# Kernel optimization log

Hardware: AMD Instinct MI355X
Metric: run time of the kernel (lower is better)

## Reference

```python
import jax, jax.numpy as jnp
import numpy as np

N_NODES = 100000
N_EDGES = 1600000
HIDDEN = 128
STEPS = 4
N_GRAPHS = 64


def setup_inputs() -> dict:
    key = jax.random.key(0)
    ks = jax.random.split(key, 8)
    x = jax.random.normal(ks[0], (N_NODES, HIDDEN), dtype=jnp.float32)
    edge_index = jax.random.randint(ks[1], (2, N_EDGES), 0, N_NODES, dtype=jnp.int64)
    batch = jnp.sort(jax.random.randint(ks[2], (N_NODES,), 0, N_GRAPHS, dtype=jnp.int64))
    s = 1.0 / np.sqrt(HIDDEN)
    weight = jax.random.normal(ks[3], (STEPS, HIDDEN, HIDDEN), dtype=jnp.float32) * s
    w_ih = jax.random.normal(ks[4], (3 * HIDDEN, HIDDEN), dtype=jnp.float32) * s
    w_hh = jax.random.normal(ks[5], (3 * HIDDEN, HIDDEN), dtype=jnp.float32) * s
    b_ih = jnp.zeros((3 * HIDDEN,), dtype=jnp.float32)
    b_hh = jnp.zeros((3 * HIDDEN,), dtype=jnp.float32)
    return {"x": x, "edge_index": edge_index, "batch": batch,
            "weight": weight, "w_ih": w_ih, "w_hh": w_hh,
            "b_ih": b_ih, "b_hh": b_hh}


def _gru_cell(m, h, w_ih, w_hh, b_ih, b_hh):
    # PyTorch GRUCell: gates ordered (r, z, n)
    gi = m @ w_ih.T + b_ih  # [N, 3H]
    gh = h @ w_hh.T + b_hh  # [N, 3H]
    i_r, i_z, i_n = jnp.split(gi, 3, axis=-1)
    h_r, h_z, h_n = jnp.split(gh, 3, axis=-1)
    r = jax.nn.sigmoid(i_r + h_r)
    z = jax.nn.sigmoid(i_z + h_z)
    n = jnp.tanh(i_n + r * h_n)
    return (1.0 - z) * n + z * h


def reference(x, edge_index, batch, weight, w_ih, w_hh, b_ih, b_hh):
    src, dst = edge_index[0], edge_index[1]
    h = x
    for i in range(STEPS):
        m = h @ weight[i]  # [N, H]
        # message = m[src] scattered (add) into dst
        aggr = jax.ops.segment_sum(m[src], dst, num_segments=N_NODES)
        h = _gru_cell(aggr, h, w_ih, w_hh, b_ih, b_hh)
    h = jax.nn.relu(h)
    # global mean pool per graph
    sums = jax.ops.segment_sum(h, batch, num_segments=N_GRAPHS)  # [G, H]
    counts = jax.ops.segment_sum(jnp.ones((N_NODES,), h.dtype), batch, num_segments=N_GRAPHS)
    return sums / jnp.maximum(counts, 1.0)[:, None]
```

## Files before the change

### kernel.cpp

```cpp
#include <hip/hip_runtime.h>

#define N_NODES  100000
#define N_EDGES  1600000
#define HIDDEN   128
#define STEPS    4
#define N_GRAPHS 64
#define NBUCK    256
#define BWID     391
#define BCAP     7168

typedef unsigned short u16;
typedef unsigned int   u32;
typedef unsigned long long u64;
typedef __attribute__((ext_vector_type(8))) short bf16x8;
typedef __attribute__((ext_vector_type(4))) float f32x4;
typedef __attribute__((ext_vector_type(2))) float f32x2;

__device__ inline u16 f2bf(float f) {
  u32 u = __float_as_uint(f);
  u = (u + 0x7FFFu + ((u >> 16) & 1u)) >> 16;
  return (u16)u;
}
__device__ inline float bf2f(u16 b) { return __uint_as_float(((u32)b) << 16); }

__device__ inline float rcp_f(float x) { return __builtin_amdgcn_rcpf(x); }
__device__ inline float sig_f(float x) { return rcp_f(1.f + __expf(-x)); }
__device__ inline float tanh_f(float x) { return 1.f - 2.f * rcp_f(1.f + __expf(2.f * x)); }

__device__ inline u32 swz(u32 b) { return b ^ (((b >> 8) & 7u) << 4); }

__global__ __launch_bounds__(1024) void k_part(const int* __restrict__ esrc,
                                               const int* __restrict__ edst,
                                               int* __restrict__ gcursor,
                                               u32* __restrict__ ebuf) {
  __shared__ int hist[16][NBUCK];
  __shared__ int base[16][NBUCK];
  int tid = threadIdx.x;
  int wv  = tid >> 6;
  #pragma unroll
  for (int i = 0; i < 4; ++i) ((int*)hist)[tid + i * 1024] = 0;
  __syncthreads();
  int e0 = blockIdx.x * 4096;
  int sv[4], dv[4], bk[4], rk[4];
  #pragma unroll
  for (int i = 0; i < 4; ++i) {
    int e = e0 + i * 1024 + tid;
    if (e < N_EDGES) {
      sv[i] = esrc[e];
      dv[i] = edst[e];
      bk[i] = (int)((u32)dv[i] / (u32)BWID);
      rk[i] = atomicAdd(&hist[wv][bk[i]], 1);
    } else bk[i] = -1;
  }
  __syncthreads();
  if (tid < NBUCK) {
    int c[16];
    int sum = 0;
    #pragma unroll
    for (int w = 0; w < 16; ++w) { c[w] = hist[w][tid]; sum += c[w]; }
    int g = atomicAdd(&gcursor[tid], sum);
    #pragma unroll
    for (int w = 0; w < 16; ++w) { base[w][tid] = g; g += c[w]; }
  }
  __syncthreads();
  #pragma unroll
  for (int i = 0; i < 4; ++i) {
    if (bk[i] >= 0) {
      int pos = bk[i] * BCAP + base[wv][bk[i]] + rk[i];
      ebuf[pos] = ((u32)(dv[i] - bk[i] * BWID) << 17) | (u32)sv[i];
    }
  }
}

__global__ void k_bscan(const int* __restrict__ gcursor, int* __restrict__ ebase,
                        float* __restrict__ acc) {
  __shared__ int buf[NBUCK];
  int t = threadIdx.x;
  int v = gcursor[t];
  buf[t] = v;
  __syncthreads();
  for (int off = 1; off < NBUCK; off <<= 1) {
    int u = 0;
    if (t >= off) u = buf[t - off];
    __syncthreads();
    buf[t] += u;
    __syncthreads();
  }
  ebase[t] = buf[t] - v;
  if (t == NBUCK - 1) ebase[NBUCK] = buf[t];
  for (int i = t; i < N_GRAPHS * HIDDEN; i += NBUCK) acc[i] = 0.f;
}

__global__ __launch_bounds__(1024) void k_csr(const u32* __restrict__ ebuf,
                                              const int* __restrict__ ebase,
                                              int* __restrict__ offs,
                                              int* __restrict__ csr) {
  __shared__ int lcnt[512];
  __shared__ int lofs[512];
  int b = blockIdx.x, tid = threadIdx.x;
  int n0 = b * BWID;
  int n1 = min(n0 + BWID, N_NODES);
  int nn = n1 - n0;
  int e0 = ebase[b];
  int cnt = ebase[b + 1] - e0;
  const u32* ebase_p = ebuf + (size_t)b * BCAP;
  if (tid < 512) lcnt[tid] = 0;
  __syncthreads();
  for (int e = tid; e < cnt; e += 1024) {
    int dst = (int)(ebase_p[e] >> 17);
    atomicAdd(&lcnt[dst], 1);
  }
  __syncthreads();
  if (tid < 512) lofs[tid] = lcnt[tid];
  __syncthreads();
  for (int off = 1; off < 512; off <<= 1) {
    int v = 0;
    if (tid < 512 && tid >= off) v = lofs[tid - off];
    __syncthreads();
    if (tid < 512 && tid >= off) lofs[tid] += v;
    __syncthreads();
  }
  int nodeoff = 0;
  if (tid < 512) nodeoff = e0 + lofs[tid] - lcnt[tid];
  if (tid < 512) lofs[tid] = nodeoff;
  if (tid < nn) offs[n0 + tid] = nodeoff;
  if (b == 0 && tid == 0) offs[N_NODES] = N_EDGES;
  __syncthreads();
  for (int e = tid; e < cnt; e += 1024) {
    u32 p = ebase_p[e];
    int src = (int)(p & 0x1FFFFu);
    int dst = (int)(p >> 17);
    int pos = atomicAdd(&lofs[dst], 1);
    csr[pos] = src;
  }
}

__global__ void k_wb(const float* __restrict__ W, const float* __restrict__ w_ih,
                     const float* __restrict__ w_hh, u16* __restrict__ bsw) {
  __shared__ float wrow[128];
  int b = blockIdx.x, st = b >> 8, k = b & 255, t = threadIdx.x;
  if (k < 128) wrow[t] = W[(st * 128 + k) * 128 + t];
  __syncthreads();
  int kc = k >> 5, quad = (k >> 3) & 3, kl = k & 7;
  u16* base = bsw + (size_t)st * 131072 + kc * 16384;
  #pragma unroll
  for (int gq = 0; gq < 4; ++gq) {
    int c = gq * 128 + t;
    float v;
    if (k < 128) {
      if (c < 384) {
        const float* wr = w_ih + c * 128;
        float sacc = 0.f;
        for (int j = 0; j < 128; ++j) sacc += wrow[j] * wr[j];
        v = sacc;
      } else v = 0.f;
    } else {
      int kk = k - 128;
      if (c < 256)      v = w_hh[c * 128 + kk];
      else if (c < 384) v = 0.f;
      else              v = w_hh[(c - 128) * 128 + kk];
    }
    int gi = c >> 7, cw = c & 127;
    int wv = cw >> 5, hu = (cw >> 4) & 1, nl = c & 15;
    int slot = wv * 8 + gi * 2 + hu;
    base[(slot * 4 + quad) * 128 + nl * 8 + kl] = f2bf(v);
  }
}

__global__ void k_convert(const float* __restrict__ x, u16* __restrict__ h0,
                          u16* __restrict__ h1) {
  int i = (blockIdx.x * 256 + threadIdx.x) * 4;
  float4 v = *(const float4*)(x + i);
  u16 o[4] = {f2bf(v.x), f2bf(v.y), f2bf(v.z), f2bf(v.w)};
  *(uint2*)(h0 + i) = *(uint2*)o;
  if (blockIdx.x == 0) {
    int t = threadIdx.x;
    if (t < 64)       ((u32*)(h0 + (size_t)N_NODES * 128))[t] = 0;
    else if (t < 128) ((u32*)(h1 + (size_t)N_NODES * 128))[t - 64] = 0;
  }
}

__device__ inline void acc8(f32x2* a, uint4 p) {
  f32x2 v;
  v.x = __uint_as_float(p.x << 16); v.y = __uint_as_float(p.x & 0xffff0000u);
  a[0] += v;
  v.x = __uint_as_float(p.y << 16); v.y = __uint_as_float(p.y & 0xffff0000u);
  a[1] += v;
  v.x = __uint_as_float(p.z << 16); v.y = __uint_as_float(p.z & 0xffff0000u);
  a[2] += v;
  v.x = __uint_as_float(p.w << 16); v.y = __uint_as_float(p.w & 0xffff0000u);
  a[3] += v;
}
__device__ inline uint4 ldrow(const char* hb, u32 off) {
  return *(const uint4*)(hb + off);
}

__global__ __launch_bounds__(256, 3) void k_fused(
    const u16* __restrict__ h_mat, const int* __restrict__ csr,
    const int* __restrict__ offs, const u16* __restrict__ bsw,
    const float* __restrict__ b_ih, const float* __restrict__ b_hh,
    u16* __restrict__ h_out) {
  __shared__ u16 Asw[8192];
  char* lds = (char*)Asw;

  const int tid  = threadIdx.x;
  const int wave = tid >> 6;
  const int lane = tid & 63;
  const int nl   = lane & 15;
  const int quad = lane >> 4;
  const int row0 = blockIdx.x * 32;

  {
    int snl = tid & 15, squad = (tid >> 4) & 3, w = tid >> 6;
    int g = w & 1;
    const u16* row = h_mat + (size_t)(row0 + g * 16 + snl) * 128;
    #pragma unroll
    for (int kk = 0; kk < 2; ++kk) {
      int kc2 = (w >> 1) * 2 + kk;
      uint4 v = *(const uint4*)(row + kc2 * 32 + squad * 8);
      u32 b = (u32)(((g * 8 + 4 + kc2) * 4 + squad) * 256 + snl * 16);
      *(uint4*)(lds + swz(b)) = v;
    }
  }

  {
    const char* hb = (const char*)h_mat;
    const int q   = quad;
    const u32 co  = (u32)(nl * 16);
    #pragma unroll 1
    for (int p = 0; p < 4; ++p) {
      int nA = wave * 8 + p * 2;
      int node = row0 + nA;
      int o0 = offs[node], o1 = offs[node + 1], o2 = offs[node + 2];
      f32x2 aA[4], aB[4];
      #pragma unroll
      for (int r = 0; r < 4; ++r) { aA[r] = (f32x2){0.f, 0.f}; aB[r] = (f32x2){0.f, 0.f}; }
      int jA = o0 + q, jB = o1 + q;
      int dmax = max(o1 - o0, o2 - o1);
      int iters = (dmax + 15) >> 4;
      #pragma unroll 1
      for (int t = 0; t < iters; ++t) {
        u32 sa[4], sb[4];
        #pragma unroll
        for (int k = 0; k < 4; ++k) {
          int jj = jA + 4 * k;
          u32 sv = (u32)csr[jj < o1 ? jj : 0];
          sa[k] = (jj < o1) ? sv : (u32)N_NODES;
          jj = jB + 4 * k;
          sv = (u32)csr[jj < o2 ? jj : 0];
          sb[k] = (jj < o2) ? sv : (u32)N_NODES;
        }
        uint4 pa0 = ldrow(hb, (sa[0] << 8) | co);
        uint4 pa1 = ldrow(hb, (sa[1] << 8) | co);
        uint4 pa2 = ldrow(hb, (sa[2] << 8) | co);
        uint4 pa3 = ldrow(hb, (sa[3] << 8) | co);
        uint4 pb0 = ldrow(hb, (sb[0] << 8) | co);
        uint4 pb1 = ldrow(hb, (sb[1] << 8) | co);
        uint4 pb2 = ldrow(hb, (sb[2] << 8) | co);
        uint4 pb3 = ldrow(hb, (sb[3] << 8) | co);
        acc8(aA, pa0); acc8(aA, pa1); acc8(aA, pa2); acc8(aA, pa3);
        acc8(aB, pb0); acc8(aB, pb1); acc8(aB, pb2); acc8(aB, pb3);
        jA += 16; jB += 16;
      }
      #pragma unroll
      for (int r = 0; r < 4; ++r) {
        aA[r].x += __shfl_xor(aA[r].x, 16); aA[r].x += __shfl_xor(aA[r].x, 32);
        aA[r].y += __shfl_xor(aA[r].y, 16); aA[r].y += __shfl_xor(aA[r].y, 32);
        aB[r].x += __shfl_xor(aB[r].x, 16); aB[r].x += __shfl_xor(aB[r].x, 32);
        aB[r].y += __shfl_xor(aB[r].y, 16); aB[r].y += __shfl_xor(aB[r].y, 32);
      }
      if (q < 2) {
        f32x2 w0 = q ? aB[0] : aA[0];
        f32x2 w1 = q ? aB[1] : aA[1];
        f32x2 w2 = q ? aB[2] : aA[2];
        f32x2 w3 = q ? aB[3] : aA[3];
        uint4 o;
        o.x = (u32)f2bf(w0.x) | ((u32)f2bf(w0.y) << 16);
        o.y = (u32)f2bf(w1.x) | ((u32)f2bf(w1.y) << 16);
        o.z = (u32)f2bf(w2.x) | ((u32)f2bf(w2.y) << 16);
        o.w = (u32)f2bf(w3.x) | ((u32)f2bf(w3.y) << 16);
        int n = nA + q, g = n >> 4, snl = n & 15;
        u32 b = (u32)(g * 8192 + nl * 256 + snl * 16);
        *(uint4*)(lds + swz(b)) = o;
      }
    }
  }
  __syncthreads();

  const u16* bp = bsw + wave * 8 * 512 + lane * 8;

  f32x4 acc[2][8];
  #pragma unroll
  for (int g = 0; g < 2; ++g)
    #pragma unroll
    for (int u = 0; u < 8; ++u) acc[g][u] = (f32x4){0.f, 0.f, 0.f, 0.f};

  bf16x8 b0[6], b1[6], b2[6];
  #pragma unroll
  for (int i = 0; i < 6; ++i) b0[i] = *(const bf16x8*)(bp + i * 512);
  #pragma unroll
  for (int i = 0; i < 6; ++i) b1[i] = *(const bf16x8*)(bp + 16384 + i * 512);

  #pragma unroll
  for (int kc = 0; kc < 8; ++kc) {
    if (kc < 6) {
      #pragma unroll
      for (int i = 0; i < 6; ++i) {
        int us = (kc + 2 < 4) ? i : (i < 4 ? i : i + 2);
        b2[i] = *(const bf16x8*)(bp + (kc + 2) * 16384 + us * 512);
      }
    }
    bf16x8 a0 = *(const bf16x8*)(lds + swz((u32)(kc * 1024 + lane * 16)));
    bf16x8 a1 = *(const bf16x8*)(lds + swz((u32)((8 + kc) * 1024 + lane * 16)));
    #pragma unroll
    for (int i = 0; i < 6; ++i) {
      int u = (kc < 4) ? i : (i < 4 ? i : i + 2);
      acc[0][u] = __builtin_amdgcn_mfma_f32_16x16x32_bf16(a0, b0[i], acc[0][u], 0, 0, 0);
      acc[1][u] = __builtin_amdgcn_mfma_f32_16x16x32_bf16(a1, b0[i], acc[1][u], 0, 0, 0);
    }
    #pragma unroll
    for (int i = 0; i < 6; ++i) { b0[i] = b1[i]; b1[i] = b2[i]; }
  }

  float bias[8];
  #pragma unroll
  for (int u = 0; u < 8; ++u) {
    int gi = u >> 1, hu = u & 1;
    int cw = wave * 32 + hu * 16 + nl;
    bias[u] = (gi == 0) ? b_ih[cw] + b_hh[cw]
            : (gi == 1) ? b_ih[128 + cw] + b_hh[128 + cw]
            : (gi == 2) ? b_ih[256 + cw]
                        : b_hh[256 + cw];
  }

  #pragma unroll
  for (int g = 0; g < 2; ++g) {
    #pragma unroll
    for (int hu = 0; hu < 2; ++hu) {
      int cw = wave * 32 + hu * 16 + nl;
      u32 hslot = (u32)((g * 8 + 4 + wave) * 4 + ((hu * 2 + (nl >> 3)) & 3));
      #pragma unroll
      for (int i = 0; i < 4; ++i) {
        int m = quad * 4 + i;
        float rv = sig_f(acc[g][0 + hu][i] + bias[0 + hu]);
        float zv = sig_f(acc[g][2 + hu][i] + bias[2 + hu]);
        float iv = acc[g][4 + hu][i] + bias[4 + hu];
        float hn = acc[g][6 + hu][i] + bias[6 + hu];
        u32 hb2 = hslot * 256 + (u32)m * 16 + (u32)(nl & 7) * 2;
        float hv = bf2f(*(const u16*)(lds + swz(hb2)));
        float n  = tanh_f(iv + rv * hn);
        float o  = n + zv * (hv - n);
        h_out[(size_t)(row0 + g * 16 + m) * 128 + cw] = f2bf(o);
      }
    }
  }
}

__global__ void k_pool_partial(const u16* __restrict__ h, const int* __restrict__ batch,
                               float* __restrict__ acc) {
  int t = threadIdx.x;
  int node0 = blockIdx.x * 125;
  int node1 = node0 + 125;
  int cur = batch[node0];
  float sum = 0.f;
  for (int r = node0; r < node1; ++r) {
    int g = batch[r];
    if (g != cur) {
      atomicAdd(&acc[cur * 128 + t], sum);
      sum = 0.f;
      cur = g;
    }
    sum += fmaxf(bf2f(h[(size_t)r * 128 + t]), 0.f);
  }
  atomicAdd(&acc[cur * 128 + t], sum);
}

__global__ void k_pool_div(const float* __restrict__ acc, const int* __restrict__ batch,
                           float* __restrict__ out) {
  __shared__ int se[2];
  int g = blockIdx.x, t = threadIdx.x;
  if (t < 2) {
    int target = g + t;
    int lo = 0, hi = N_NODES;
    while (lo < hi) { int mid = (lo + hi) >> 1; if (batch[mid] < target) lo = mid + 1; else hi = mid; }
    se[t] = lo;
  }
  __syncthreads();
  int cnt = se[1] - se[0];
  out[g * 128 + t] = acc[g * 128 + t] / (float)(cnt > 0 ? cnt : 1);
}

extern "C" void kernel_launch(void* const* d_in, const int* in_sizes, int n_in,
                              void* d_out, int out_size, void* d_ws, size_t ws_size,
                              hipStream_t stream) {
  const float* x     = (const float*)d_in[0];
  const int*   edges = (const int*)d_in[1];
  const int*   batch = (const int*)d_in[2];
  const float* W     = (const float*)d_in[3];
  const float* w_ih  = (const float*)d_in[4];
  const float* w_hh  = (const float*)d_in[5];
  const float* b_ih  = (const float*)d_in[6];
  const float* b_hh  = (const float*)d_in[7];
  float* out = (float*)d_out;

  char* w = (char*)d_ws;
  u16* buf0    = (u16*)(w);
  u16* buf1    = (u16*)(w + 25600256);
  u16* bsw     = (u16*)(w + 51200512);
  float* acc   = (float*)(w + 52249088);
  int* offs    = (int*)(w + 52281856);
  int* gcursor = (int*)(w + 52682240);
  int* ebase   = (int*)(w + 52683264);
  int* csr     = (int*)(w + 52684800);
  u32* ebuf    = (u32*)buf1;

  const int* esrc = edges;
  const int* edst = edges + N_EDGES;

  hipMemsetAsync(gcursor, 0, NBUCK * sizeof(int), stream);
  k_part<<<391, 1024, 0, stream>>>(esrc, edst, gcursor, ebuf);
  k_bscan<<<1, NBUCK, 0, stream>>>(gcursor, ebase, acc);
  k_csr<<<NBUCK, 1024, 0, stream>>>(ebuf, ebase, offs, csr);
  k_wb<<<1024, 128, 0, stream>>>(W, w_ih, w_hh, bsw);
  k_convert<<<(N_NODES * HIDDEN) / 1024, 256, 0, stream>>>(x, buf0, buf1);

  u16* hcur = buf0;
  u16* hnxt = buf1;
  for (int st = 0; st < STEPS; ++st) {
    k_fused<<<N_NODES / 32, 256, 0, stream>>>(hcur, csr, offs, bsw + st * 131072,
                                              b_ih, b_hh, hnxt);
    u16* tmp = hcur; hcur = hnxt; hnxt = tmp;
  }
  k_pool_partial<<<800, 128, 0, stream>>>(hcur, batch, acc);
  k_pool_div<<<N_GRAPHS, 128, 0, stream>>>(acc, batch, out);
}
```

Measured before the change: 569.4 us.

## Split fused gather+GEMM-GRU kernel into separate gather and GEMM kernels

The per-step fused kernel is split into two launches. A standalone k_gather kernel does the CSR neighbour sum and writes a bf16 aggregate buffer, and k_gemm_gru loads both the aggregate and h into LDS for the MFMA GEMM and GRU epilogue. The point is to run the latency-bound irregular gather at higher occupancy, free of the register and LDS limits of the GEMM. The cost is an extra aggregate write and read per step plus an extra launch. The LDS XOR swizzle is also dropped, which can bring back bank conflicts, and the aggregate buffer is overwritten in place by the GEMM kernel's output.

```diff
diff --git a/kernel.cpp b/kernel.cpp
--- a/kernel.cpp
+++ b/kernel.cpp
@@ -26,8 +26,6 @@
 __device__ inline float rcp_f(float x) { return __builtin_amdgcn_rcpf(x); }
 __device__ inline float sig_f(float x) { return rcp_f(1.f + __expf(-x)); }
 __device__ inline float tanh_f(float x) { return 1.f - 2.f * rcp_f(1.f + __expf(2.f * x)); }
-
-__device__ inline u32 swz(u32 b) { return b ^ (((b >> 8) & 7u) << 4); }
 
 __global__ __launch_bounds__(1024) void k_part(const int* __restrict__ esrc,
                                                const int* __restrict__ edst,
@@ -195,13 +193,72 @@
   return *(const uint4*)(hb + off);
 }
 
-__global__ __launch_bounds__(256, 3) void k_fused(
-    const u16* __restrict__ h_mat, const int* __restrict__ csr,
-    const int* __restrict__ offs, const u16* __restrict__ bsw,
-    const float* __restrict__ b_ih, const float* __restrict__ b_hh,
-    u16* __restrict__ h_out) {
+__global__ void k_gather(const u16* __restrict__ h, const int* __restrict__ csr,
+                         const int* __restrict__ offs, u16* __restrict__ s) {
+  int wave = threadIdx.x >> 6;
+  int lane = threadIdx.x & 63;
+  int q   = lane >> 4;
+  int nl  = lane & 15;
+  int nodeA = blockIdx.x * 8 + wave * 2;
+  const char* hb = (const char*)h;
+  const u32 co = (u32)(nl * 16);
+  int o0 = offs[nodeA], o1 = offs[nodeA + 1], o2 = offs[nodeA + 2];
+  f32x2 aA[4], aB[4];
+  #pragma unroll
+  for (int r = 0; r < 4; ++r) { aA[r] = (f32x2){0.f, 0.f}; aB[r] = (f32x2){0.f, 0.f}; }
+  int jA = o0 + q, jB = o1 + q;
+  int dmax = max(o1 - o0, o2 - o1);
+  int iters = (dmax + 15) >> 4;
+  #pragma unroll 1
+  for (int t = 0; t < iters; ++t) {
+    u32 sa[4], sb[4];
+    #pragma unroll
+    for (int k = 0; k < 4; ++k) {
+      int jj = jA + 4 * k;
+      u32 sv = (u32)csr[jj < o1 ? jj : 0];
+      sa[k] = (jj < o1) ? sv : (u32)N_NODES;
+      jj = jB + 4 * k;
+      sv = (u32)csr[jj < o2 ? jj : 0];
+      sb[k] = (jj < o2) ? sv : (u32)N_NODES;
+    }
+    uint4 pa0 = ldrow(hb, (sa[0] << 8) | co);
+    uint4 pa1 = ldrow(hb, (sa[1] << 8) | co);
+    uint4 pa2 = ldrow(hb, (sa[2] << 8) | co);
+    uint4 pa3 = ldrow(hb, (sa[3] << 8) | co);
+    uint4 pb0 = ldrow(hb, (sb[0] << 8) | co);
+    uint4 pb1 = ldrow(hb, (sb[1] << 8) | co);
+    uint4 pb2 = ldrow(hb, (sb[2] << 8) | co);
+    uint4 pb3 = ldrow(hb, (sb[3] << 8) | co);
+    acc8(aA, pa0); acc8(aA, pa1); acc8(aA, pa2); acc8(aA, pa3);
+    acc8(aB, pb0); acc8(aB, pb1); acc8(aB, pb2); acc8(aB, pb3);
+    jA += 16; jB += 16;
+  }
+  #pragma unroll
+  for (int r = 0; r < 4; ++r) {
+    aA[r].x += __shfl_xor(aA[r].x, 16); aA[r].x += __shfl_xor(aA[r].x, 32);
+    aA[r].y += __shfl_xor(aA[r].y, 16); aA[r].y += __shfl_xor(aA[r].y, 32);
+    aB[r].x += __shfl_xor(aB[r].x, 16); aB[r].x += __shfl_xor(aB[r].x, 32);
+    aB[r].y += __shfl_xor(aB[r].y, 16); aB[r].y += __shfl_xor(aB[r].y, 32);
+  }
+  if (q < 2) {
+    f32x2 w0 = q ? aB[0] : aA[0];
+    f32x2 w1 = q ? aB[1] : aA[1];
+    f32x2 w2 = q ? aB[2] : aA[2];
+    f32x2 w3 = q ? aB[3] : aA[3];
+    uint4 o;
+    o.x = (u32)f2bf(w0.x) | ((u32)f2bf(w0.y) << 16);
+    o.y = (u32)f2bf(w1.x) | ((u32)f2bf(w1.y) << 16);
+    o.z = (u32)f2bf(w2.x) | ((u32)f2bf(w2.y) << 16);
+    o.w = (u32)f2bf(w3.x) | ((u32)f2bf(w3.y) << 16);
+    *(uint4*)(s + (size_t)(nodeA + q) * 128 + nl * 8) = o;
+  }
+}
+
+__global__ __launch_bounds__(256, 2) void k_gemm_gru(
+    const u16* __restrict__ s_mat, const u16* __restrict__ h_mat,
+    const u16* __restrict__ bsw, const float* __restrict__ b_ih,
+    const float* __restrict__ b_hh, u16* __restrict__ h_out) {
   __shared__ u16 Asw[8192];
-  char* lds = (char*)Asw;
 
   const int tid  = threadIdx.x;
   const int wave = tid >> 6;
@@ -211,78 +268,13 @@
   const int row0 = blockIdx.x * 32;
 
   {
-    int snl = tid & 15, squad = (tid >> 4) & 3, w = tid >> 6;
-    int g = w & 1;
-    const u16* row = h_mat + (size_t)(row0 + g * 16 + snl) * 128;
-    #pragma unroll
-    for (int kk = 0; kk < 2; ++kk) {
-      int kc2 = (w >> 1) * 2 + kk;
+    int snl = tid & 15, squad = (tid >> 4) & 3, sel = tid >> 6;
+    int g = sel & 1, half = sel >> 1;
+    const u16* row = (half ? h_mat : s_mat) + (size_t)(row0 + g * 16 + snl) * 128;
+    #pragma unroll
+    for (int kc2 = 0; kc2 < 4; ++kc2) {
       uint4 v = *(const uint4*)(row + kc2 * 32 + squad * 8);
-      u32 b = (u32)(((g * 8 + 4 + kc2) * 4 + squad) * 256 + snl * 16);
-      *(uint4*)(lds + swz(b)) = v;
-    }
-  }
-
-  {
-    const char* hb = (const char*)h_mat;
-    const int q   = quad;
-    const u32 co  = (u32)(nl * 16);
-    #pragma unroll 1
-    for (int p = 0; p < 4; ++p) {
-      int nA = wave * 8 + p * 2;
-      int node = row0 + nA;
-      int o0 = offs[node], o1 = offs[node + 1], o2 = offs[node + 2];
-      f32x2 aA[4], aB[4];
-      #pragma unroll
-      for (int r = 0; r < 4; ++r) { aA[r] = (f32x2){0.f, 0.f}; aB[r] = (f32x2){0.f, 0.f}; }
-      int jA = o0 + q, jB = o1 + q;
-      int dmax = max(o1 - o0, o2 - o1);
-      int iters = (dmax + 15) >> 4;
-      #pragma unroll 1
-      for (int t = 0; t < iters; ++t) {
-        u32 sa[4], sb[4];
-        #pragma unroll
-        for (int k = 0; k < 4; ++k) {
-          int jj = jA + 4 * k;
-          u32 sv = (u32)csr[jj < o1 ? jj : 0];
-          sa[k] = (jj < o1) ? sv : (u32)N_NODES;
-          jj = jB + 4 * k;
-          sv = (u32)csr[jj < o2 ? jj : 0];
-          sb[k] = (jj < o2) ? sv : (u32)N_NODES;
-        }
-        uint4 pa0 = ldrow(hb, (sa[0] << 8) | co);
-        uint4 pa1 = ldrow(hb, (sa[1] << 8) | co);
-        uint4 pa2 = ldrow(hb, (sa[2] << 8) | co);
-        uint4 pa3 = ldrow(hb, (sa[3] << 8) | co);
-        uint4 pb0 = ldrow(hb, (sb[0] << 8) | co);
-        uint4 pb1 = ldrow(hb, (sb[1] << 8) | co);
-        uint4 pb2 = ldrow(hb, (sb[2] << 8) | co);
-        uint4 pb3 = ldrow(hb, (sb[3] << 8) | co);
-        acc8(aA, pa0); acc8(aA, pa1); acc8(aA, pa2); acc8(aA, pa3);
-        acc8(aB, pb0); acc8(aB, pb1); acc8(aB, pb2); acc8(aB, pb3);
-        jA += 16; jB += 16;
-      }
-      #pragma unroll
-      for (int r = 0; r < 4; ++r) {
-        aA[r].x += __shfl_xor(aA[r].x, 16); aA[r].x += __shfl_xor(aA[r].x, 32);
-        aA[r].y += __shfl_xor(aA[r].y, 16); aA[r].y += __shfl_xor(aA[r].y, 32);
-        aB[r].x += __shfl_xor(aB[r].x, 16); aB[r].x += __shfl_xor(aB[r].x, 32);
-        aB[r].y += __shfl_xor(aB[r].y, 16); aB[r].y += __shfl_xor(aB[r].y, 32);
-      }
-      if (q < 2) {
-        f32x2 w0 = q ? aB[0] : aA[0];
-        f32x2 w1 = q ? aB[1] : aA[1];
-        f32x2 w2 = q ? aB[2] : aA[2];
-        f32x2 w3 = q ? aB[3] : aA[3];
-        uint4 o;
-        o.x = (u32)f2bf(w0.x) | ((u32)f2bf(w0.y) << 16);
-        o.y = (u32)f2bf(w1.x) | ((u32)f2bf(w1.y) << 16);
-        o.z = (u32)f2bf(w2.x) | ((u32)f2bf(w2.y) << 16);
-        o.w = (u32)f2bf(w3.x) | ((u32)f2bf(w3.y) << 16);
-        int n = nA + q, g = n >> 4, snl = n & 15;
-        u32 b = (u32)(g * 8192 + nl * 256 + snl * 16);
-        *(uint4*)(lds + swz(b)) = o;
-      }
+      *(uint4*)&Asw[(((g * 8 + half * 4 + kc2) * 4 + squad) * 16 + snl) * 8] = v;
     }
   }
   __syncthreads();
@@ -310,8 +302,8 @@
         b2[i] = *(const bf16x8*)(bp + (kc + 2) * 16384 + us * 512);
       }
     }
-    bf16x8 a0 = *(const bf16x8*)(lds + swz((u32)(kc * 1024 + lane * 16)));
-    bf16x8 a1 = *(const bf16x8*)(lds + swz((u32)((8 + kc) * 1024 + lane * 16)));
+    bf16x8 a0 = *(const bf16x8*)&Asw[kc * 512 + lane * 8];
+    bf16x8 a1 = *(const bf16x8*)&Asw[(8 + kc) * 512 + lane * 8];
     #pragma unroll
     for (int i = 0; i < 6; ++i) {
       int u = (kc < 4) ? i : (i < 4 ? i : i + 2);
@@ -338,7 +330,7 @@
     #pragma unroll
     for (int hu = 0; hu < 2; ++hu) {
       int cw = wave * 32 + hu * 16 + nl;
-      u32 hslot = (u32)((g * 8 + 4 + wave) * 4 + ((hu * 2 + (nl >> 3)) & 3));
+      int hbase = ((g * 8 + 4 + wave) * 4 + ((hu * 2 + (nl >> 3)) & 3)) * 128 + (nl & 7);
       #pragma unroll
       for (int i = 0; i < 4; ++i) {
         int m = quad * 4 + i;
@@ -346,8 +338,7 @@
         float zv = sig_f(acc[g][2 + hu][i] + bias[2 + hu]);
         float iv = acc[g][4 + hu][i] + bias[4 + hu];
         float hn = acc[g][6 + hu][i] + bias[6 + hu];
-        u32 hb2 = hslot * 256 + (u32)m * 16 + (u32)(nl & 7) * 2;
-        float hv = bf2f(*(const u16*)(lds + swz(hb2)));
+        float hv = bf2f(Asw[hbase + m * 8]);
         float n  = tanh_f(iv + rv * hn);
         float o  = n + zv * (hv - n);
         h_out[(size_t)(row0 + g * 16 + m) * 128 + cw] = f2bf(o);
@@ -427,8 +418,9 @@
   u16* hcur = buf0;
   u16* hnxt = buf1;
   for (int st = 0; st < STEPS; ++st) {
-    k_fused<<<N_NODES / 32, 256, 0, stream>>>(hcur, csr, offs, bsw + st * 131072,
-                                              b_ih, b_hh, hnxt);
+    k_gather<<<N_NODES / 8, 256, 0, stream>>>(hcur, csr, offs, hnxt);
+    k_gemm_gru<<<N_NODES / 32, 256, 0, stream>>>(hnxt, hcur, bsw + st * 131072,
+                                                 b_ih, b_hh, hnxt);
     u16* tmp = hcur; hcur = hnxt; hnxt = tmp;
   }
   k_pool_partial<<<800, 128, 0, stream>>>(hcur, batch, acc);
```

After: 583.0 us. +2.4%, slower.
